# Performance work log

Measured on AMD Instinct MI355X. Metric: run time of the kernel, lower is better.

## Reference

```python
import jax, jax.numpy as jnp
import numpy as np
from jax import lax

DN = ('NCHW', 'OIHW', 'NCHW')


def _conv(x, w, padding, groups=1):
    return lax.conv_general_dilated(
        x, w, window_strides=(1, 1), padding=padding,
        dimension_numbers=DN, feature_group_count=groups)


def _l2_normalize(t, axis=-1, eps=1e-12):
    # matches torch.nn.functional.normalize: x / max(||x||, eps)
    n = jnp.sqrt(jnp.sum(t * t, axis=axis, keepdims=True))
    return t / jnp.maximum(n, eps)


def _topk_masked_softmax(attn, k):
    # attn: [b, H, C, C]; keep exactly the top-k entries per row (by index,
    # matching torch.topk + scatter), set rest to -inf, then softmax.
    C = attn.shape[-1]
    idx = lax.top_k(attn, k)[1]                              # [b, H, C, k]
    mask = jax.nn.one_hot(idx, C, dtype=jnp.bool_).any(-2)   # [b, H, C, C]
    return jax.nn.softmax(jnp.where(mask, attn, -jnp.inf), axis=-1)


def setup_inputs() -> dict:
    key = jax.random.key(0)
    ks = jax.random.split(key, 4)
    dim, heads, b, h, w = 64, 2, 8, 256, 256
    x = jax.random.normal(ks[0], (b, dim, h, w), dtype=jnp.float32)
    w_qkv = jax.random.normal(ks[1], (3 * dim, dim, 1, 1), dtype=jnp.float32) * 0.05
    w_dw = jax.random.normal(ks[2], (3 * dim, 1, 3, 3), dtype=jnp.float32) * 0.05
    w_proj = jax.random.normal(ks[3], (dim, dim, 1, 1), dtype=jnp.float32) * 0.05
    temperature = jnp.ones((heads, 1, 1), dtype=jnp.float32)
    a1 = jnp.array([0.2], dtype=jnp.float32)
    a2 = jnp.array([0.2], dtype=jnp.float32)
    a3 = jnp.array([0.2], dtype=jnp.float32)
    return {"x": x, "w_qkv": w_qkv, "w_dw": w_dw, "w_proj": w_proj,
            "temperature": temperature, "a1": a1, "a2": a2, "a3": a3}


def reference(x, w_qkv, w_dw, w_proj, temperature, a1, a2, a3):
    heads = temperature.shape[0]
    b, c, h, w = x.shape
    qkv = _conv(x, w_qkv, padding=[(0, 0), (0, 0)])
    qkv = _conv(qkv, w_dw, padding=[(1, 1), (1, 1)], groups=3 * c)
    q, k, v = jnp.split(qkv, 3, axis=1)

    def to_heads(t):  # b (head C) h w -> b head C (h w)
        return t.reshape(b, heads, c // heads, h * w)

    q, k, v = to_heads(q), to_heads(k), to_heads(v)
    q = _l2_normalize(q)
    k = _l2_normalize(k)

    C = c // heads
    attn = jnp.einsum('bhcn,bhdn->bhcd', q, k) * temperature  # [b, H, C, C]

    attn1 = _topk_masked_softmax(attn, C // 2)
    attn2 = _topk_masked_softmax(attn, (C * 2) // 3)
    attn3 = _topk_masked_softmax(attn, (C * 3) // 4)

    out = (jnp.einsum('bhcd,bhdn->bhcn', attn1, v) * a1
           + jnp.einsum('bhcd,bhdn->bhcn', attn2, v) * a2
           + jnp.einsum('bhcd,bhdn->bhcn', attn3, v) * a3)

    out = out.reshape(b, c, h, w)
    return _conv(out, w_proj, padding=[(0, 0), (0, 0)])
```

## Files before the change

### kernel.cpp

```cpp
#include <hip/hip_runtime.h>
#include <math.h>

constexpr int B_   = 8;
constexpr int CIN  = 64;
constexpr int C3   = 192;
constexpr int HWID = 256;
constexpr long long NPIX = 65536;

constexpr int K3_CHUNKS = 128;
constexpr int K3_CELLS  = 1088;

constexpr size_t SZ_QKV1B = (size_t)C3 * NPIX;
constexpr size_t SZ_QKB   = (size_t)128 * NPIX;
constexpr size_t OFF_QKV1B = 0;
constexpr size_t OFF_QKB   = OFF_QKV1B + SZ_QKV1B;
constexpr size_t OFF_GRAM  = OFF_QKB + SZ_QKB;
constexpr size_t SZ_GRAM   = (size_t)B_ * 2 * 32 * 32;
constexpr size_t OFF_NORM  = OFF_GRAM + SZ_GRAM;
constexpr size_t SZ_NORM   = (size_t)B_ * 2 * 64;
constexpr size_t OFF_M     = OFF_NORM + SZ_NORM;
constexpr size_t SZ_M      = (size_t)B_ * 64 * 64;
constexpr size_t OFF_PART  = OFF_M + SZ_M;
constexpr size_t SZ_PART   = (size_t)B_ * 2 * K3_CHUNKS * K3_CELLS;

constexpr int LSTR = 68;

__global__ __launch_bounds__(256) void k1_qkv1x1(const float* __restrict__ x,
                                                 const float* __restrict__ wqkv,
                                                 float* __restrict__ qkv1, int b) {
  __shared__ __align__(16) float xs[64][LSTR];
  __shared__ __align__(16) float Wt[64][LSTR];
  const int t = threadIdx.x;
  const long long n0 = (long long)blockIdx.x * 64;
  const int oc0 = blockIdx.y * 64;
  const float* xb = x + (size_t)b * CIN * NPIX;

  {
    const int p4 = (t & 15) * 4;
#pragma unroll
    for (int r = 0; r < 4; ++r) {
      const int ic = (t >> 4) + 16 * r;
      const float4 v = *(const float4*)(xb + (size_t)ic * NPIX + n0 + p4);
      *(float4*)(&xs[ic][p4]) = v;
    }
    const int ic4 = (t & 15) * 4;
#pragma unroll
    for (int r = 0; r < 4; ++r) {
      const int ocl = (t >> 4) + 16 * r;
      const float4 w = *(const float4*)(wqkv + (size_t)(oc0 + ocl) * 64 + ic4);
      Wt[ic4 + 0][ocl] = w.x;
      Wt[ic4 + 1][ocl] = w.y;
      Wt[ic4 + 2][ocl] = w.z;
      Wt[ic4 + 3][ocl] = w.w;
    }
  }
  __syncthreads();

  const int ocl0 = (t >> 4) * 4;
  const int p0   = (t & 15) * 4;
  float acc[4][4] = {};
#pragma unroll 4
  for (int j = 0; j < 64; ++j) {
    const float4 a  = *(const float4*)(&Wt[j][ocl0]);
    const float4 bq = *(const float4*)(&xs[j][p0]);
    const float av[4] = {a.x, a.y, a.z, a.w};
    const float bv[4] = {bq.x, bq.y, bq.z, bq.w};
#pragma unroll
    for (int i = 0; i < 4; ++i)
#pragma unroll
      for (int p = 0; p < 4; ++p)
        acc[i][p] = fmaf(av[i], bv[p], acc[i][p]);
  }
#pragma unroll
  for (int i = 0; i < 4; ++i) {
    float4 o;
    o.x = acc[i][0]; o.y = acc[i][1]; o.z = acc[i][2]; o.w = acc[i][3];
    *(float4*)(qkv1 + (size_t)(oc0 + ocl0 + i) * NPIX + n0 + p0) = o;
  }
}

__global__ __launch_bounds__(256) void k2_dwconv(const float* __restrict__ qkv1,
                                                 const float* __restrict__ wdw,
                                                 float* __restrict__ qkbuf,
                                                 float* __restrict__ vout) {
  const int r0 = blockIdx.x * 4;
  const int ch = blockIdx.y;
  const int t  = threadIdx.x;
  __shared__ __align__(16) float sm[6][256];
  const float* p = qkv1 + (size_t)ch * NPIX;

  for (int idx = t; idx < 384; idx += 256) {
    const int rr = idx >> 6;
    const int c4 = (idx & 63) * 4;
    const int gr = r0 - 1 + rr;
    float4 v = make_float4(0.f, 0.f, 0.f, 0.f);
    if (gr >= 0 && gr < HWID) v = *(const float4*)(p + (size_t)gr * HWID + c4);
    *(float4*)(&sm[rr][c4]) = v;
  }
  float w[9];
#pragma unroll
  for (int i = 0; i < 9; ++i) w[i] = wdw[ch * 9 + i];
  __syncthreads();

  const int col = t;
  float cell[6][3];
#pragma unroll
  for (int rr = 0; rr < 6; ++rr) {
    cell[rr][0] = (col > 0)   ? sm[rr][col - 1] : 0.f;
    cell[rr][1] = sm[rr][col];
    cell[rr][2] = (col < 255) ? sm[rr][col + 1] : 0.f;
  }
  float* dst = (ch < 128) ? (qkbuf + (size_t)ch * NPIX)
                          : (vout + (size_t)(ch - 128) * NPIX);
#pragma unroll
  for (int k = 0; k < 4; ++k) {
    float acc = 0.f;
#pragma unroll
    for (int ky = 0; ky < 3; ++ky)
#pragma unroll
      for (int kx = 0; kx < 3; ++kx)
        acc = fmaf(w[ky * 3 + kx], cell[k + ky][kx], acc);
    dst[(size_t)(r0 + k) * HWID + col] = acc;
  }
}

__global__ __launch_bounds__(1024) void k3_gram(const float* __restrict__ qkbuf,
                                                float* __restrict__ part, int b) {
  const int chunk = blockIdx.x;
  const int h = blockIdx.y;
  const int t = threadIdx.x;
  const int nt = t & 15;
  const int tile = t >> 4;
  const int c0 = (tile & 7) * 4;
  const int d0 = (tile >> 3) * 4;
  const bool do_qn = (d0 == 0);
  const bool do_kn = (c0 == 0);
  const float* qb = qkbuf + (size_t)(h * 32) * NPIX;
  const float* kb = qkbuf + (size_t)(64 + h * 32) * NPIX;

  float acc[4][4] = {};
  float qn[4] = {}, kn[4] = {};
  const long long n0 = (long long)chunk * 512 + nt * 4;
#pragma unroll 2
  for (int s = 0; s < 8; ++s) {
    const long long n = n0 + (long long)s * 64;
    float4 qv[4], kv[4];
#pragma unroll
    for (int i = 0; i < 4; ++i)
      qv[i] = *(const float4*)(qb + (size_t)(c0 + i) * NPIX + n);
#pragma unroll
    for (int j = 0; j < 4; ++j)
      kv[j] = *(const float4*)(kb + (size_t)(d0 + j) * NPIX + n);
#pragma unroll
    for (int i = 0; i < 4; ++i)
#pragma unroll
      for (int j = 0; j < 4; ++j) {
        float a = acc[i][j];
        a = fmaf(qv[i].x, kv[j].x, a);
        a = fmaf(qv[i].y, kv[j].y, a);
        a = fmaf(qv[i].z, kv[j].z, a);
        a = fmaf(qv[i].w, kv[j].w, a);
        acc[i][j] = a;
      }
    if (do_qn) {
#pragma unroll
      for (int i = 0; i < 4; ++i) {
        float a = qn[i];
        a = fmaf(qv[i].x, qv[i].x, a);
        a = fmaf(qv[i].y, qv[i].y, a);
        a = fmaf(qv[i].z, qv[i].z, a);
        a = fmaf(qv[i].w, qv[i].w, a);
        qn[i] = a;
      }
    }
    if (do_kn) {
#pragma unroll
      for (int j = 0; j < 4; ++j) {
        float a = kn[j];
        a = fmaf(kv[j].x, kv[j].x, a);
        a = fmaf(kv[j].y, kv[j].y, a);
        a = fmaf(kv[j].z, kv[j].z, a);
        a = fmaf(kv[j].w, kv[j].w, a);
        kn[j] = a;
      }
    }
  }

  float* pb = part + (((size_t)(b * 2 + h)) * K3_CHUNKS + chunk) * K3_CELLS;
#pragma unroll
  for (int i = 0; i < 4; ++i)
#pragma unroll
    for (int j = 0; j < 4; ++j) {
      float v = acc[i][j];
      v += __shfl_xor(v, 1); v += __shfl_xor(v, 2);
      v += __shfl_xor(v, 4); v += __shfl_xor(v, 8);
      if (nt == 0) pb[(c0 + i) * 32 + (d0 + j)] = v;
    }
  if (do_qn) {
#pragma unroll
    for (int i = 0; i < 4; ++i) {
      float v = qn[i];
      v += __shfl_xor(v, 1); v += __shfl_xor(v, 2);
      v += __shfl_xor(v, 4); v += __shfl_xor(v, 8);
      if (nt == 0) pb[1024 + c0 + i] = v;
    }
  }
  if (do_kn) {
#pragma unroll
    for (int j = 0; j < 4; ++j) {
      float v = kn[j];
      v += __shfl_xor(v, 1); v += __shfl_xor(v, 2);
      v += __shfl_xor(v, 4); v += __shfl_xor(v, 8);
      if (nt == 0) pb[1056 + d0 + j] = v;
    }
  }
}

__global__ __launch_bounds__(256) void k3_reduce(const float* __restrict__ part,
                                                 float* __restrict__ gram,
                                                 float* __restrict__ norms) {
  const int e = blockIdx.x * 256 + threadIdx.x;
  const int bh = e / K3_CELLS;
  const int cell = e - bh * K3_CELLS;
  const float* p = part + ((size_t)bh * K3_CHUNKS) * K3_CELLS + cell;
  float s0 = 0.f, s1 = 0.f;
#pragma unroll 4
  for (int ch = 0; ch < K3_CHUNKS; ch += 2) {
    s0 += p[(size_t)ch * K3_CELLS];
    s1 += p[(size_t)(ch + 1) * K3_CELLS];
  }
  const float s = s0 + s1;
  if (cell < 1024) gram[(size_t)bh * 1024 + cell] = s;
  else             norms[(size_t)bh * 64 + (cell - 1024)] = s;
}

__global__ __launch_bounds__(256) void k4_attn(const float* __restrict__ gram,
                                               const float* __restrict__ norms,
                                               const float* __restrict__ temp,
                                               const float* __restrict__ a1,
                                               const float* __restrict__ a2,
                                               const float* __restrict__ a3,
                                               const float* __restrict__ wproj,
                                               float* __restrict__ M) {
  const int b = blockIdx.x;
  const int t = threadIdx.x;
  __shared__ float A[2][32][32];
  if (t < 64) {
    const int h = t >> 5, c = t & 31;
    const float* g = gram + (((size_t)b * 2 + h) * 32 + c) * 32;
    const float* nb = norms + ((size_t)b * 2 + h) * 64;
    const float qn = fmaxf(sqrtf(nb[c]), 1e-12f);
    const float tmph = temp[h];
    float v[32];
#pragma unroll
    for (int d = 0; d < 32; ++d) {
      const float kn = fmaxf(sqrtf(nb[32 + d]), 1e-12f);
      v[d] = g[d] / (qn * kn) * tmph;
    }
    int rank[32];
#pragma unroll
    for (int i = 0; i < 32; ++i) {
      int r = 0;
#pragma unroll
      for (int j = 0; j < 32; ++j)
        r += (v[j] > v[i]) || (v[j] == v[i] && j < i);
      rank[i] = r;
    }
    float acc[32];
#pragma unroll
    for (int d = 0; d < 32; ++d) acc[d] = 0.f;
    const float aws[3] = {a1[0], a2[0], a3[0]};
    const int kvs[3] = {16, 21, 24};
#pragma unroll 1
    for (int kk = 0; kk < 3; ++kk) {
      float mx = -3.4e38f;
#pragma unroll
      for (int d = 0; d < 32; ++d)
        if (rank[d] < kvs[kk]) mx = fmaxf(mx, v[d]);
      float s = 0.f;
#pragma unroll
      for (int d = 0; d < 32; ++d)
        if (rank[d] < kvs[kk]) s += expf(v[d] - mx);
      const float inv = aws[kk] / s;
#pragma unroll
      for (int d = 0; d < 32; ++d)
        if (rank[d] < kvs[kk]) acc[d] += expf(v[d] - mx) * inv;
    }
#pragma unroll
    for (int d = 0; d < 32; ++d) A[h][c][d] = acc[d];
  }
  __syncthreads();
  for (int e = t; e < 4096; e += 256) {
    const int oc = e >> 6, j = e & 63, h = j >> 5, d = j & 31;
    float s = 0.f;
#pragma unroll
    for (int c = 0; c < 32; ++c)
      s += wproj[oc * 64 + h * 32 + c] * A[h][c][d];
    M[(size_t)b * 4096 + e] = s;
  }
}

__global__ __launch_bounds__(256) void k5_out(float* vy,
                                              const float* __restrict__ M) {
  __shared__ __align__(16) float vs[64][LSTR];
  __shared__ __align__(16) float Mt[64][LSTR];
  const int t = threadIdx.x;
  const int b = blockIdx.y;
  const long long n0 = (long long)blockIdx.x * 64;
  float* vb = vy + (size_t)b * 64 * NPIX;
  const float* Mb = M + (size_t)b * 4096;

  {
    const int p4 = (t & 15) * 4;
#pragma unroll
    for (int r = 0; r < 4; ++r) {
      const int j = (t >> 4) + 16 * r;
      const float4 v = *(const float4*)(vb + (size_t)j * NPIX + n0 + p4);
      *(float4*)(&vs[j][p4]) = v;
    }
    const int j4 = (t & 15) * 4;
#pragma unroll
    for (int r = 0; r < 4; ++r) {
      const int oc = (t >> 4) + 16 * r;
      const float4 m = *(const float4*)(Mb + (size_t)oc * 64 + j4);
      Mt[j4 + 0][oc] = m.x;
      Mt[j4 + 1][oc] = m.y;
      Mt[j4 + 2][oc] = m.z;
      Mt[j4 + 3][oc] = m.w;
    }
  }
  __syncthreads();

  const int ocl0 = (t >> 4) * 4;
  const int p0   = (t & 15) * 4;
  float acc[4][4] = {};
#pragma unroll 4
  for (int j = 0; j < 64; ++j) {
    const float4 a  = *(const float4*)(&Mt[j][ocl0]);
    const float4 bq = *(const float4*)(&vs[j][p0]);
    const float av[4] = {a.x, a.y, a.z, a.w};
    const float bv[4] = {bq.x, bq.y, bq.z, bq.w};
#pragma unroll
    for (int i = 0; i < 4; ++i)
#pragma unroll
      for (int p = 0; p < 4; ++p)
        acc[i][p] = fmaf(av[i], bv[p], acc[i][p]);
  }
#pragma unroll
  for (int i = 0; i < 4; ++i) {
    float4 o;
    o.x = acc[i][0]; o.y = acc[i][1]; o.z = acc[i][2]; o.w = acc[i][3];
    *(float4*)(vb + (size_t)(ocl0 + i) * NPIX + n0 + p0) = o;
  }
}

extern "C" void kernel_launch(void* const* d_in, const int* in_sizes, int n_in,
                              void* d_out, int out_size, void* d_ws, size_t ws_size,
                              hipStream_t stream) {
  const float* x     = (const float*)d_in[0];
  const float* wqkv  = (const float*)d_in[1];
  const float* wdw   = (const float*)d_in[2];
  const float* wproj = (const float*)d_in[3];
  const float* temp  = (const float*)d_in[4];
  const float* a1    = (const float*)d_in[5];
  const float* a2    = (const float*)d_in[6];
  const float* a3    = (const float*)d_in[7];

  float* ws    = (float*)d_ws;
  float* qkv1b = ws + OFF_QKV1B;
  float* qkb   = ws + OFF_QKB;
  float* gram  = ws + OFF_GRAM;
  float* norms = ws + OFF_NORM;
  float* M     = ws + OFF_M;
  float* part  = ws + OFF_PART;
  float* y     = (float*)d_out;

  dim3 blk(256);
  for (int b = 0; b < B_; ++b) {
    k1_qkv1x1<<<dim3(1024, 3), blk, 0, stream>>>(x, wqkv, qkv1b, b);
    k2_dwconv<<<dim3(64, C3), blk, 0, stream>>>(
        qkv1b, wdw, qkb, y + (size_t)b * 64 * NPIX);
    k3_gram<<<dim3(K3_CHUNKS, 2), dim3(1024), 0, stream>>>(qkb, part, b);
  }
  k3_reduce<<<dim3(68), blk, 0, stream>>>(part, gram, norms);
  k4_attn<<<dim3(B_), blk, 0, stream>>>(gram, norms, temp, a1, a2, a3, wproj, M);
  k5_out<<<dim3(1024, B_), blk, 0, stream>>>(y, M);
}
```

Measured before the change: 808.2 us.

## Batch k1/k2/k3 launches across images and stream dwconv rows with register reuse

Launches the 1x1 QKV conv and depthwise conv over four images at a time, and the gram kernel over all eight images in one grid, when the workspace is large enough. This cuts the number of small launches and gives each launch more blocks to fill the GPU. The depthwise conv now processes 16 rows per block, keeping a rolling 3-row window in registers so halo rows are reloaded less often. The cost is a much larger workspace footprint, with the old per-image schedule kept as a fallback when the workspace is too small.

```diff
diff --git a/kernel.cpp b/kernel.cpp
--- a/kernel.cpp
+++ b/kernel.cpp
@@ -10,30 +10,26 @@
 constexpr int K3_CHUNKS = 128;
 constexpr int K3_CELLS  = 1088;
 
-constexpr size_t SZ_QKV1B = (size_t)C3 * NPIX;
-constexpr size_t SZ_QKB   = (size_t)128 * NPIX;
-constexpr size_t OFF_QKV1B = 0;
-constexpr size_t OFF_QKB   = OFF_QKV1B + SZ_QKV1B;
-constexpr size_t OFF_GRAM  = OFF_QKB + SZ_QKB;
-constexpr size_t SZ_GRAM   = (size_t)B_ * 2 * 32 * 32;
-constexpr size_t OFF_NORM  = OFF_GRAM + SZ_GRAM;
-constexpr size_t SZ_NORM   = (size_t)B_ * 2 * 64;
-constexpr size_t OFF_M     = OFF_NORM + SZ_NORM;
-constexpr size_t SZ_M      = (size_t)B_ * 64 * 64;
-constexpr size_t OFF_PART  = OFF_M + SZ_M;
-constexpr size_t SZ_PART   = (size_t)B_ * 2 * K3_CHUNKS * K3_CELLS;
+constexpr size_t SZ_QKV1_1B = (size_t)C3 * NPIX;
+constexpr size_t SZ_QKB_1B  = (size_t)128 * NPIX;
+constexpr size_t SZ_GRAM = (size_t)B_ * 2 * 32 * 32;
+constexpr size_t SZ_NORM = (size_t)B_ * 2 * 64;
+constexpr size_t SZ_M    = (size_t)B_ * 64 * 64;
+constexpr size_t SZ_PART = (size_t)B_ * 2 * K3_CHUNKS * K3_CELLS;
 
 constexpr int LSTR = 68;
 
 __global__ __launch_bounds__(256) void k1_qkv1x1(const float* __restrict__ x,
                                                  const float* __restrict__ wqkv,
-                                                 float* __restrict__ qkv1, int b) {
+                                                 float* __restrict__ qkv1, int b0) {
   __shared__ __align__(16) float xs[64][LSTR];
   __shared__ __align__(16) float Wt[64][LSTR];
   const int t = threadIdx.x;
+  const int lb = blockIdx.z;
   const long long n0 = (long long)blockIdx.x * 64;
   const int oc0 = blockIdx.y * 64;
-  const float* xb = x + (size_t)b * CIN * NPIX;
+  const float* xb = x + (size_t)(b0 + lb) * CIN * NPIX;
+  float* outb = qkv1 + (size_t)lb * SZ_QKV1_1B;
 
   {
     const int p4 = (t & 15) * 4;
@@ -75,21 +71,23 @@
   for (int i = 0; i < 4; ++i) {
     float4 o;
     o.x = acc[i][0]; o.y = acc[i][1]; o.z = acc[i][2]; o.w = acc[i][3];
-    *(float4*)(qkv1 + (size_t)(oc0 + ocl0 + i) * NPIX + n0 + p0) = o;
+    *(float4*)(outb + (size_t)(oc0 + ocl0 + i) * NPIX + n0 + p0) = o;
   }
 }
 
 __global__ __launch_bounds__(256) void k2_dwconv(const float* __restrict__ qkv1,
                                                  const float* __restrict__ wdw,
-                                                 float* __restrict__ qkbuf,
+                                                 float* __restrict__ qkb,
+                                                 size_t qkb_stride,
                                                  float* __restrict__ vout) {
-  const int r0 = blockIdx.x * 4;
+  const int r0 = blockIdx.x * 16;
   const int ch = blockIdx.y;
+  const int lb = blockIdx.z;
   const int t  = threadIdx.x;
-  __shared__ __align__(16) float sm[6][256];
-  const float* p = qkv1 + (size_t)ch * NPIX;
-
-  for (int idx = t; idx < 384; idx += 256) {
+  __shared__ __align__(16) float sm[18][256];
+  const float* p = qkv1 + (size_t)lb * SZ_QKV1_1B + (size_t)ch * NPIX;
+
+  for (int idx = t; idx < 18 * 64; idx += 256) {
     const int rr = idx >> 6;
     const int c4 = (idx & 63) * 4;
     const int gr = r0 - 1 + rr;
@@ -103,31 +101,35 @@
   __syncthreads();
 
   const int col = t;
-  float cell[6][3];
-#pragma unroll
-  for (int rr = 0; rr < 6; ++rr) {
-    cell[rr][0] = (col > 0)   ? sm[rr][col - 1] : 0.f;
-    cell[rr][1] = sm[rr][col];
-    cell[rr][2] = (col < 255) ? sm[rr][col + 1] : 0.f;
-  }
-  float* dst = (ch < 128) ? (qkbuf + (size_t)ch * NPIX)
-                          : (vout + (size_t)(ch - 128) * NPIX);
-#pragma unroll
-  for (int k = 0; k < 4; ++k) {
-    float acc = 0.f;
-#pragma unroll
-    for (int ky = 0; ky < 3; ++ky)
-#pragma unroll
-      for (int kx = 0; kx < 3; ++kx)
-        acc = fmaf(w[ky * 3 + kx], cell[k + ky][kx], acc);
+  const bool cl = (col > 0), cr = (col < 255);
+  float l0 = cl ? sm[0][col - 1] : 0.f, m0 = sm[0][col], r0v = cr ? sm[0][col + 1] : 0.f;
+  float l1 = cl ? sm[1][col - 1] : 0.f, m1 = sm[1][col], r1v = cr ? sm[1][col + 1] : 0.f;
+  float* dst = (ch < 128)
+                   ? (qkb + (size_t)lb * qkb_stride + (size_t)ch * NPIX)
+                   : (vout + (size_t)lb * 64 * NPIX + (size_t)(ch - 128) * NPIX);
+#pragma unroll
+  for (int k = 0; k < 16; ++k) {
+    const float l2 = cl ? sm[k + 2][col - 1] : 0.f;
+    const float m2 = sm[k + 2][col];
+    const float r2v = cr ? sm[k + 2][col + 1] : 0.f;
+    float acc = w[0] * l0;
+    acc = fmaf(w[1], m0, acc);  acc = fmaf(w[2], r0v, acc);
+    acc = fmaf(w[3], l1, acc);  acc = fmaf(w[4], m1, acc);
+    acc = fmaf(w[5], r1v, acc); acc = fmaf(w[6], l2, acc);
+    acc = fmaf(w[7], m2, acc);  acc = fmaf(w[8], r2v, acc);
     dst[(size_t)(r0 + k) * HWID + col] = acc;
+    l0 = l1; m0 = m1; r0v = r1v;
+    l1 = l2; m1 = m2; r1v = r2v;
   }
 }
 
 __global__ __launch_bounds__(1024) void k3_gram(const float* __restrict__ qkbuf,
-                                                float* __restrict__ part, int b) {
+                                                size_t qkb_stride,
+                                                float* __restrict__ part, int b0) {
   const int chunk = blockIdx.x;
   const int h = blockIdx.y;
+  const int lb = blockIdx.z;
+  const int b = b0 + lb;
   const int t = threadIdx.x;
   const int nt = t & 15;
   const int tile = t >> 4;
@@ -135,8 +137,9 @@
   const int d0 = (tile >> 3) * 4;
   const bool do_qn = (d0 == 0);
   const bool do_kn = (c0 == 0);
-  const float* qb = qkbuf + (size_t)(h * 32) * NPIX;
-  const float* kb = qkbuf + (size_t)(64 + h * 32) * NPIX;
+  const float* base = qkbuf + (size_t)lb * qkb_stride;
+  const float* qb = base + (size_t)(h * 32) * NPIX;
+  const float* kb = base + (size_t)(64 + h * 32) * NPIX;
 
   float acc[4][4] = {};
   float qn[4] = {}, kn[4] = {};
@@ -365,24 +368,50 @@
   const float* a1    = (const float*)d_in[5];
   const float* a2    = (const float*)d_in[6];
   const float* a3    = (const float*)d_in[7];
-
-  float* ws    = (float*)d_ws;
-  float* qkv1b = ws + OFF_QKV1B;
-  float* qkb   = ws + OFF_QKB;
-  float* gram  = ws + OFF_GRAM;
-  float* norms = ws + OFF_NORM;
-  float* M     = ws + OFF_M;
-  float* part  = ws + OFF_PART;
-  float* y     = (float*)d_out;
+  float* y = (float*)d_out;
+  float* ws = (float*)d_ws;
+
+  const size_t ws_floats = ws_size / sizeof(float);
+  const size_t smalls = SZ_GRAM + SZ_NORM + SZ_M + SZ_PART;
+  const size_t needA = 4 * SZ_QKV1_1B + (size_t)B_ * SZ_QKB_1B + smalls;
 
   dim3 blk(256);
-  for (int b = 0; b < B_; ++b) {
-    k1_qkv1x1<<<dim3(1024, 3), blk, 0, stream>>>(x, wqkv, qkv1b, b);
-    k2_dwconv<<<dim3(64, C3), blk, 0, stream>>>(
-        qkv1b, wdw, qkb, y + (size_t)b * 64 * NPIX);
-    k3_gram<<<dim3(K3_CHUNKS, 2), dim3(1024), 0, stream>>>(qkb, part, b);
-  }
-  k3_reduce<<<dim3(68), blk, 0, stream>>>(part, gram, norms);
-  k4_attn<<<dim3(B_), blk, 0, stream>>>(gram, norms, temp, a1, a2, a3, wproj, M);
-  k5_out<<<dim3(1024, B_), blk, 0, stream>>>(y, M);
-}
+  if (ws_floats >= needA) {
+    float* qkv1  = ws;
+    float* qkb   = qkv1 + 4 * SZ_QKV1_1B;
+    float* gram  = qkb + (size_t)B_ * SZ_QKB_1B;
+    float* norms = gram + SZ_GRAM;
+    float* M     = norms + SZ_NORM;
+    float* part  = M + SZ_M;
+
+    for (int half = 0; half < 2; ++half) {
+      const int b0 = half * 4;
+      k1_qkv1x1<<<dim3(1024, 3, 4), blk, 0, stream>>>(x, wqkv, qkv1, b0);
+      k2_dwconv<<<dim3(16, C3, 4), blk, 0, stream>>>(
+          qkv1, wdw, qkb + (size_t)b0 * SZ_QKB_1B, SZ_QKB_1B,
+          y + (size_t)b0 * 64 * NPIX);
+    }
+    k3_gram<<<dim3(K3_CHUNKS, 2, B_), dim3(1024), 0, stream>>>(
+        qkb, SZ_QKB_1B, part, 0);
+    k3_reduce<<<dim3(68), blk, 0, stream>>>(part, gram, norms);
+    k4_attn<<<dim3(B_), blk, 0, stream>>>(gram, norms, temp, a1, a2, a3, wproj, M);
+    k5_out<<<dim3(1024, B_), blk, 0, stream>>>(y, M);
+  } else {
+    float* qkv1  = ws;
+    float* qkb   = qkv1 + SZ_QKV1_1B;
+    float* gram  = qkb + SZ_QKB_1B;
+    float* norms = gram + SZ_GRAM;
+    float* M     = norms + SZ_NORM;
+    float* part  = M + SZ_M;
+
+    for (int b = 0; b < B_; ++b) {
+      k1_qkv1x1<<<dim3(1024, 3, 1), blk, 0, stream>>>(x, wqkv, qkv1, b);
+      k2_dwconv<<<dim3(16, C3, 1), blk, 0, stream>>>(
+          qkv1, wdw, qkb, 0, y + (size_t)b * 64 * NPIX);
+      k3_gram<<<dim3(K3_CHUNKS, 2, 1), dim3(1024), 0, stream>>>(qkb, 0, part, b);
+    }
+    k3_reduce<<<dim3(68), blk, 0, stream>>>(part, gram, norms);
+    k4_attn<<<dim3(B_), blk, 0, stream>>>(gram, norms, temp, a1, a2, a3, wproj, M);
+    k5_out<<<dim3(1024, B_), blk, 0, stream>>>(y, M);
+  }
+}
```

New measurement: 761.8 us. -5.7%, faster.
